# Performance work log

Hardware: AMD Instinct MI355X
Metric: run time of the kernel (lower is better)

Reference implementation:

```python
import jax, jax.numpy as jnp
import numpy as np

H = 512      # hidden_size
DB = 128     # dim_B
DC = 16      # dim_C
N = 2048     # batch


def setup_inputs() -> dict:
    key = jax.random.key(0)
    ks = jax.random.split(key, 8)
    u = lambda k, shp: jax.random.uniform(k, shp, jnp.float32, -0.1, 0.1)
    return {
        "input_data": jax.random.normal(ks[0], (N, H), jnp.float32),
        "W1": u(ks[1], (H, 2 * H)), "b1": jnp.zeros((2 * H,), jnp.float32),
        "W2": u(ks[2], (2 * H, 3 * H)), "b2": jnp.zeros((3 * H,), jnp.float32),
        "Wh": u(ks[3], (3 * H, 3 * H)), "bh": jnp.zeros((3 * H,), jnp.float32),
        "W3": u(ks[4], (3 * H, 2 * H)), "b3": jnp.zeros((2 * H,), jnp.float32),
        "W4": u(ks[5], (2 * H, H)), "b4": jnp.zeros((H,), jnp.float32),
        "Wo": u(ks[6], (H + DB, 1)), "bo": jnp.zeros((1,), jnp.float32),
        "T": jax.random.normal(ks[7], (H, DB * DC), jnp.float32),
    }


def _minibatch_disc(Ms):
    # Ms: [N, B, C]. out[i, b] = sum_j exp(-sum_c |Ms[i,b,c]-Ms[j,b,c]|)
    # Sequential map over B keeps the [N, N, C] intermediate bounded.
    def per_b(m):  # m: [N, C]
        d = jnp.sum(jnp.abs(m[:, None, :] - m[None, :, :]), axis=-1)  # [N, N]
        return jnp.sum(jnp.exp(-d), axis=1)  # [N]
    return jax.lax.map(per_b, jnp.transpose(Ms, (1, 0, 2))).T  # [N, B]


def reference(input_data, W1, b1, W2, b2, Wh, bh, W3, b3, W4, b4, Wo, bo, T):
    x = jax.nn.relu(input_data @ W1 + b1)
    x = jax.nn.relu(x @ W2 + b2)
    x = jax.nn.relu(x @ Wh + bh)  # dropout(p=0) == identity
    x = jax.nn.relu(x @ W3 + b3)
    feature = jax.nn.relu(x @ W4 + b4)          # [N, H]
    Ms = (feature @ T).reshape(-1, DB, DC)      # [N, B, C]
    out_T = _minibatch_disc(Ms)                 # [N, B]
    logits = jnp.concatenate([feature, out_T], axis=1) @ Wo + bo
    return feature, jax.nn.sigmoid(logits)
```

## Files before the change

### kernel.cpp

```cpp
#include <hip/hip_runtime.h>
#include <hip/hip_bf16.h>
#include <math.h>

#define NROWS 2048
#define HD 512
#define DBx 128

typedef __attribute__((ext_vector_type(8)))  short bf16x8;
typedef __attribute__((ext_vector_type(4)))  float f32x4;
typedef __attribute__((ext_vector_type(16))) float f32x16;

__device__ inline unsigned pack2_bf16(float a, float b) {
    union { __hip_bfloat162 h; unsigned u; } cv;
    cv.h = __float22bfloat162_rn(make_float2(a, b));
    return cv.u;
}
__device__ inline unsigned short pack1_bf16(float a) {
    union { __hip_bfloat16 h; unsigned short u; } cv;
    cv.h = __float2bfloat16(a);
    return cv.u;
}

__global__ __launch_bounds__(256) void conv_bf16_kernel(const float* __restrict__ in,
                                                        unsigned short* __restrict__ out,
                                                        int n4) {
    for (int idx = blockIdx.x * 256 + threadIdx.x; idx < n4; idx += gridDim.x * 256) {
        const float4 v = *reinterpret_cast<const float4*>(in + (size_t)idx * 4);
        uint2 o;
        o.x = pack2_bf16(v.x, v.y);
        o.y = pack2_bf16(v.z, v.w);
        *reinterpret_cast<uint2*>(out + (size_t)idx * 4) = o;
    }
}

struct TransArgs {
    const float* src[6];
    unsigned short* dst[6];
    int K[6], M[6], t0[6];
};

__global__ __launch_bounds__(256) void trans_all_kernel(TransArgs a) {
    const int id = blockIdx.x;
    int m = 0;
    #pragma unroll
    for (int q = 1; q < 6; ++q) if (id >= a.t0[q]) m = q;
    const int local = id - a.t0[m];
    const int M = a.M[m], K = a.K[m];
    const int ntm = M >> 5;
    const int mt = local % ntm;
    const int kt = local / ntm;
    const float* W = a.src[m];
    unsigned short* Wt = a.dst[m];

    __shared__ float tile[32][33];
    const int t  = threadIdx.x;
    const int tr = t >> 3;
    const int tc = t & 7;
    const int k0 = kt * 32;
    const int m0 = mt * 32;

    const float4 v = *reinterpret_cast<const float4*>(&W[(size_t)(k0 + tr) * M + m0 + tc * 4]);
    tile[tr][tc * 4 + 0] = v.x;
    tile[tr][tc * 4 + 1] = v.y;
    tile[tr][tc * 4 + 2] = v.z;
    tile[tr][tc * 4 + 3] = v.w;
    __syncthreads();

    const float x = tile[tc * 4 + 0][tr];
    const float y = tile[tc * 4 + 1][tr];
    const float z = tile[tc * 4 + 2][tr];
    const float w = tile[tc * 4 + 3][tr];
    uint2 o;
    o.x = pack2_bf16(x, y);
    o.y = pack2_bf16(z, w);
    *reinterpret_cast<uint2*>(&Wt[(size_t)(m0 + tr) * K + k0 + tc * 4]) = o;
}

template<int WRITE_BF16, int WRITE_F32, int RELU, int BIAS, int MSB>
__global__ __launch_bounds__(256) void gemm64_kernel(const unsigned short* __restrict__ Abf,
                                                     const unsigned short* __restrict__ Bt,
                                                     const float* __restrict__ bias,
                                                     unsigned short* __restrict__ Cbf,
                                                     float* __restrict__ Cf,
                                                     int K, int M) {
    __shared__ unsigned short As[2][64 * 64];
    __shared__ unsigned short Bs[2][64 * 64];

    const int t    = threadIdx.x;
    const int lane = t & 63;
    const int wv   = t >> 6;
    const int wm   = wv & 1;
    const int wn   = wv >> 1;
    const int row0 = blockIdx.y * 64;
    const int col0 = blockIdx.x * 64;
    const int gl_r = lane >> 3;
    const int gl_c = lane & 7;

    f32x4 acc[2][2] = {};

    auto STAGE = [&](int bufi, int kt) {
        #pragma unroll
        for (int q = 0; q < 2; ++q) {
            const int r = wv * 16 + q * 8 + gl_r;
            const unsigned short* srcA = Abf + (size_t)(row0 + r) * K + kt + 8 * (gl_c ^ (r & 7));
            __builtin_amdgcn_global_load_lds(
                (const __attribute__((address_space(1))) void*)srcA,
                (__attribute__((address_space(3))) void*)(&As[bufi][(wv * 16 + q * 8) * 64]),
                16, 0, 0);
            const unsigned short* srcB = Bt + (size_t)(col0 + r) * K + kt + 8 * (gl_c ^ (r & 7));
            __builtin_amdgcn_global_load_lds(
                (const __attribute__((address_space(1))) void*)srcB,
                (__attribute__((address_space(3))) void*)(&Bs[bufi][(wv * 16 + q * 8) * 64]),
                16, 0, 0);
        }
    };

    const int nkt = K >> 6;
    STAGE(0, 0);
    __syncthreads();
    int buf = 0;
    for (int kt = 0; kt < nkt; ++kt) {
        if (kt + 1 < nkt) STAGE(buf ^ 1, (kt + 1) * 64);
        const int lm = lane & 15;
        const int kg = lane >> 4;
        #pragma unroll
        for (int ks = 0; ks < 2; ++ks) {
            bf16x8 af[2], bfr[2];
            #pragma unroll
            for (int fi = 0; fi < 2; ++fi) {
                const int r  = wm * 32 + fi * 16 + lm;
                const int ch = (kg + 4 * ks) ^ (r & 7);
                af[fi] = *reinterpret_cast<const bf16x8*>((const char*)&As[buf][0] + r * 128 + ch * 16);
            }
            #pragma unroll
            for (int fj = 0; fj < 2; ++fj) {
                const int n  = wn * 32 + fj * 16 + lm;
                const int ch = (kg + 4 * ks) ^ (n & 7);
                bfr[fj] = *reinterpret_cast<const bf16x8*>((const char*)&Bs[buf][0] + n * 128 + ch * 16);
            }
            #pragma unroll
            for (int fi = 0; fi < 2; ++fi)
                #pragma unroll
                for (int fj = 0; fj < 2; ++fj)
                    acc[fi][fj] = __builtin_amdgcn_mfma_f32_16x16x32_bf16(
                        af[fi], bfr[fj], acc[fi][fj], 0, 0, 0);
        }
        __syncthreads();
        buf ^= 1;
    }

    const int lm = lane & 15;
    const int lq = lane >> 4;
    #pragma unroll
    for (int fj = 0; fj < 2; ++fj) {
        const int col = col0 + wn * 32 + fj * 16 + lm;
        const float bv = BIAS ? bias[col] : 0.f;
        #pragma unroll
        for (int fi = 0; fi < 2; ++fi) {
            #pragma unroll
            for (int r = 0; r < 4; ++r) {
                const int row = row0 + wm * 32 + fi * 16 + lq * 4 + r;
                float v = acc[fi][fj][r] + bv;
                if (RELU) v = fmaxf(v, 0.f);
                if (WRITE_F32)  Cf[(size_t)row * M + col] = v;
                if (WRITE_BF16) {
                    if (MSB)
                        Cbf[(size_t)(col >> 4) * (NROWS * 16) + (size_t)row * 16 + (col & 15)] = pack1_bf16(v);
                    else
                        Cbf[(size_t)row * M + col] = pack1_bf16(v);
                }
            }
        }
    }
}

__global__ __launch_bounds__(256) void norms_kernel(const float* __restrict__ Ms,
                                                    float* __restrict__ nrm,
                                                    float* __restrict__ oT) {
    const int g = blockIdx.x * 256 + threadIdx.x;
    const int i = g >> 7;
    const int b = g & 127;
    const float* p = Ms + (size_t)i * 2048 + b * 16;
    float s = 0.f;
    #pragma unroll
    for (int c = 0; c < 16; c += 4) {
        const float4 v = *reinterpret_cast<const float4*>(p + c);
        s += v.x * v.x + v.y * v.y + v.z * v.z + v.w * v.w;
    }
    nrm[(size_t)b * 2048 + i] = 0.495f * s;
    oT[g] = 0.f;
}

__global__ __launch_bounds__(512) void mbdisc32_kernel(const float* __restrict__ Ms,
                                                       const unsigned short* __restrict__ Msb,
                                                       const float* __restrict__ nrm,
                                                       float* __restrict__ outT) {
    extern __shared__ char smem[];
    float* Nlds = (float*)(smem + 32768);

    const int t    = threadIdx.x;
    const int lane = t & 63;
    const int w    = t >> 6;
    const int b    = blockIdx.y;
    const int jh   = blockIdx.z;
    const int cl   = lane & 31;
    const int hk   = lane >> 5;
    const int jbase = jh * 1024;

    const unsigned short* Mb = Msb + (size_t)b * NROWS * 16;
    const float* nb = nrm + (size_t)b * NROWS;

    #pragma unroll
    for (int q = 0; q < 4; ++q) {
        const int slot = q * 512 + t;
        const int h = slot >> 10, jj = slot & 1023;
        const unsigned short* src = Mb + (size_t)(jbase + jj) * 16 + h * 8;
        __builtin_amdgcn_global_load_lds(
            (const __attribute__((address_space(1))) void*)src,
            (__attribute__((address_space(3))) void*)(smem + (size_t)(q * 512 + w * 64) * 16),
            16, 0, 0);
    }
    if (w < 4) {
        const float* src = nb + jbase + (w * 64 + lane) * 4;
        __builtin_amdgcn_global_load_lds(
            (const __attribute__((address_space(1))) void*)src,
            (__attribute__((address_space(3))) void*)(smem + 32768 + (size_t)(w * 64) * 16),
            16, 0, 0);
    }

    bf16x8 afc[4];
    #pragma unroll
    for (int ic = 0; ic < 4; ++ic) {
        const int i0 = blockIdx.x * 1024 + w * 128 + ic * 32;
        afc[ic] = *reinterpret_cast<const bf16x8*>(Mb + (size_t)(i0 + cl) * 16 + hk * 8);
    }
    __syncthreads();

    const char* mrow = smem + hk * 16384;

    #pragma unroll
    for (int ic = 0; ic < 4; ++ic) {
        const int i0 = blockIdx.x * 1024 + w * 128 + ic * 32;
        const bf16x8 af = afc[ic];

        f32x16 cI;
        #pragma unroll
        for (int q = 0; q < 4; ++q) {
            const float4 v = *reinterpret_cast<const float4*>(nb + i0 + 4 * hk + 8 * q);
            cI[4 * q + 0] = 725.f - v.x; cI[4 * q + 1] = 725.f - v.y;
            cI[4 * q + 2] = 725.f - v.z; cI[4 * q + 3] = 725.f - v.w;
        }

        #pragma unroll 2
        for (int j0 = 0; j0 < 1024; j0 += 64) {
            const float nj0 = Nlds[j0 + cl];
            const float nj1 = Nlds[j0 + 32 + cl];
            const bf16x8 b0 = *reinterpret_cast<const bf16x8*>(mrow + (size_t)(j0 + cl) * 16);
            const bf16x8 b1 = *reinterpret_cast<const bf16x8*>(mrow + (size_t)(j0 + 32 + cl) * 16);
            const f32x16 a0 = __builtin_amdgcn_mfma_f32_32x32x16_bf16(af, b0, cI, 0, 0, 0);
            const f32x16 a1 = __builtin_amdgcn_mfma_f32_32x32x16_bf16(af, b1, cI, 0, 0, 0);

            float x0 = fmaxf(fmaxf(a0[0], a0[1]), fmaxf(a0[2], a0[3]));
            float x1 = fmaxf(fmaxf(a0[4], a0[5]), fmaxf(a0[6], a0[7]));
            float x2 = fmaxf(fmaxf(a0[8], a0[9]), fmaxf(a0[10], a0[11]));
            float x3 = fmaxf(fmaxf(a0[12], a0[13]), fmaxf(a0[14], a0[15]));
            const float mx0 = fmaxf(fmaxf(x0, x1), fmaxf(x2, x3));
            float y0 = fmaxf(fmaxf(a1[0], a1[1]), fmaxf(a1[2], a1[3]));
            float y1 = fmaxf(fmaxf(a1[4], a1[5]), fmaxf(a1[6], a1[7]));
            float y2 = fmaxf(fmaxf(a1[8], a1[9]), fmaxf(a1[10], a1[11]));
            float y3 = fmaxf(fmaxf(a1[12], a1[13]), fmaxf(a1[14], a1[15]));
            const float mx1 = fmaxf(fmaxf(y0, y1), fmaxf(y2, y3));

            if (__any(fmaxf(mx0 - nj0, mx1 - nj1) > 0.f)) {
                #pragma unroll
                for (int r = 0; r < 16; ++r) {
                    if (a0[r] > nj0) {
                        const int i = i0 + (r & 3) + 8 * (r >> 2) + 4 * hk;
                        const int j = jbase + j0 + cl;
                        const float* pi = Ms + (size_t)i * 2048 + b * 16;
                        const float* pj = Ms + (size_t)j * 2048 + b * 16;
                        float s = 0.f;
                        #pragma unroll
                        for (int cc = 0; cc < 16; cc += 4) {
                            const float4 x = *reinterpret_cast<const float4*>(pi + cc);
                            const float4 y = *reinterpret_cast<const float4*>(pj + cc);
                            s += (fabsf(x.x - y.x) + fabsf(x.y - y.y)) +
                                 (fabsf(x.z - y.z) + fabsf(x.w - y.w));
                        }
                        atomicAdd(&outT[(size_t)i * DBx + b], __expf(-s));
                    }
                }
                #pragma unroll
                for (int r = 0; r < 16; ++r) {
                    if (a1[r] > nj1) {
                        const int i = i0 + (r & 3) + 8 * (r >> 2) + 4 * hk;
                        const int j = jbase + j0 + 32 + cl;
                        const float* pi = Ms + (size_t)i * 2048 + b * 16;
                        const float* pj = Ms + (size_t)j * 2048 + b * 16;
                        float s = 0.f;
                        #pragma unroll
                        for (int cc = 0; cc < 16; cc += 4) {
                            const float4 x = *reinterpret_cast<const float4*>(pi + cc);
                            const float4 y = *reinterpret_cast<const float4*>(pj + cc);
                            s += (fabsf(x.x - y.x) + fabsf(x.y - y.y)) +
                                 (fabsf(x.z - y.z) + fabsf(x.w - y.w));
                        }
                        atomicAdd(&outT[(size_t)i * DBx + b], __expf(-s));
                    }
                }
            }
        }
    }
}

__global__ __launch_bounds__(256) void logits_kernel(const float* __restrict__ feat,
                                                     const float* __restrict__ outT,
                                                     const float* __restrict__ Wo,
                                                     const float* __restrict__ bo,
                                                     float* __restrict__ out2) {
    const int row = blockIdx.x;
    const int t   = threadIdx.x;
    float p = 0.f;
    for (int k = t; k < HD + DBx; k += 256) {
        const float x = (k < HD) ? feat[(size_t)row * HD + k]
                                 : outT[(size_t)row * DBx + (k - HD)];
        p += x * Wo[k];
    }
    #pragma unroll
    for (int off = 32; off; off >>= 1) p += __shfl_down(p, off, 64);
    __shared__ float ws[4];
    if ((t & 63) == 0) ws[t >> 6] = p;
    __syncthreads();
    if (t == 0) {
        const float s = ws[0] + ws[1] + ws[2] + ws[3] + bo[0];
        out2[row] = 1.f / (1.f + __expf(-s));
    }
}

extern "C" void kernel_launch(void* const* d_in, const int* in_sizes, int n_in,
                              void* d_out, int out_size, void* d_ws, size_t ws_size,
                              hipStream_t stream) {
    const float* input = (const float*)d_in[0];
    const float* W1 = (const float*)d_in[1];
    const float* b1 = (const float*)d_in[2];
    const float* W2 = (const float*)d_in[3];
    const float* b2 = (const float*)d_in[4];
    const float* Wh = (const float*)d_in[5];
    const float* bh = (const float*)d_in[6];
    const float* W3 = (const float*)d_in[7];
    const float* b3 = (const float*)d_in[8];
    const float* W4 = (const float*)d_in[9];
    const float* b4 = (const float*)d_in[10];
    const float* Wo = (const float*)d_in[11];
    const float* bo = (const float*)d_in[12];
    const float* T  = (const float*)d_in[13];

    unsigned short* inbf  = (unsigned short*)d_ws;
    unsigned short* W1t   = inbf  + (size_t)2048 * 512;
    unsigned short* W2t   = W1t   + (size_t)1024 * 512;
    unsigned short* Wht   = W2t   + (size_t)1536 * 1024;
    unsigned short* W3t   = Wht   + (size_t)1536 * 1536;
    unsigned short* W4t   = W3t   + (size_t)1024 * 1536;
    unsigned short* Tt    = W4t   + (size_t)512 * 1024;
    unsigned short* slabA = Tt    + (size_t)2048 * 512;
    unsigned short* slabB = slabA + (size_t)2048 * 1536;
    float* Ms  = (float*)(slabB + (size_t)2048 * 1536);
    float* oT  = Ms + (size_t)2048 * 2048;
    float* nrm = oT + (size_t)2048 * 128;
    unsigned short* Msb = inbf;

    unsigned short* x1bf   = slabA;
    unsigned short* x2bf   = slabB;
    unsigned short* x3bf   = slabA;
    unsigned short* x4bf   = slabB;
    unsigned short* featbf = slabA;

    float* feat = (float*)d_out;
    float* out2 = feat + (size_t)NROWS * HD;

    const dim3 blk(256);

    conv_bf16_kernel<<<1024, blk, 0, stream>>>(input, inbf, 2048 * 512 / 4);

    TransArgs ta;
    ta.src[0] = W1; ta.dst[0] = W1t; ta.K[0] =  512; ta.M[0] = 1024; ta.t0[0] = 0;
    ta.src[1] = W2; ta.dst[1] = W2t; ta.K[1] = 1024; ta.M[1] = 1536; ta.t0[1] = 512;
    ta.src[2] = Wh; ta.dst[2] = Wht; ta.K[2] = 1536; ta.M[2] = 1536; ta.t0[2] = 2048;
    ta.src[3] = W3; ta.dst[3] = W3t; ta.K[3] = 1536; ta.M[3] = 1024; ta.t0[3] = 4352;
    ta.src[4] = W4; ta.dst[4] = W4t; ta.K[4] = 1024; ta.M[4] =  512; ta.t0[4] = 5888;
    ta.src[5] = T;  ta.dst[5] = Tt;  ta.K[5] =  512; ta.M[5] = 2048; ta.t0[5] = 6400;
    trans_all_kernel<<<7424, blk, 0, stream>>>(ta);

    gemm64_kernel<1, 0, 1, 1, 0><<<dim3(1024 / 64, 32), blk, 0, stream>>>(inbf, W1t, b1, x1bf, nullptr, 512, 1024);
    gemm64_kernel<1, 0, 1, 1, 0><<<dim3(1536 / 64, 32), blk, 0, stream>>>(x1bf, W2t, b2, x2bf, nullptr, 1024, 1536);
    gemm64_kernel<1, 0, 1, 1, 0><<<dim3(1536 / 64, 32), blk, 0, stream>>>(x2bf, Wht, bh, x3bf, nullptr, 1536, 1536);
    gemm64_kernel<1, 0, 1, 1, 0><<<dim3(1024 / 64, 32), blk, 0, stream>>>(x3bf, W3t, b3, x4bf, nullptr, 1536, 1024);
    gemm64_kernel<1, 1, 1, 1, 0><<<dim3( 512 / 64, 32), blk, 0, stream>>>(x4bf, W4t, b4, featbf, feat, 1024, 512);
    gemm64_kernel<1, 1, 0, 0, 1><<<dim3(2048 / 64, 32), blk, 0, stream>>>(featbf, Tt, nullptr, Msb, Ms, 512, 2048);

    norms_kernel<<<1024, blk, 0, stream>>>(Ms, nrm, oT);
    mbdisc32_kernel<<<dim3(2, 128, 2), dim3(512), 36864, stream>>>(Ms, Msb, nrm, oT);

    logits_kernel<<<NROWS, blk, 0, stream>>>(feat, oT, Wo, bo, out2);
}
```

Baseline: 262.1 us.

## Exploit pairwise symmetry in minibatch discrimination and fuse input conversion into transpose

```diff
diff --git a/kernel.cpp b/kernel.cpp
--- a/kernel.cpp
+++ b/kernel.cpp
@@ -19,18 +19,6 @@
     union { __hip_bfloat16 h; unsigned short u; } cv;
     cv.h = __float2bfloat16(a);
     return cv.u;
-}
-
-__global__ __launch_bounds__(256) void conv_bf16_kernel(const float* __restrict__ in,
-                                                        unsigned short* __restrict__ out,
-                                                        int n4) {
-    for (int idx = blockIdx.x * 256 + threadIdx.x; idx < n4; idx += gridDim.x * 256) {
-        const float4 v = *reinterpret_cast<const float4*>(in + (size_t)idx * 4);
-        uint2 o;
-        o.x = pack2_bf16(v.x, v.y);
-        o.y = pack2_bf16(v.z, v.w);
-        *reinterpret_cast<uint2*>(out + (size_t)idx * 4) = o;
-    }
 }
 
 struct TransArgs {
@@ -38,9 +26,22 @@
     unsigned short* dst[6];
     int K[6], M[6], t0[6];
 };
-
-__global__ __launch_bounds__(256) void trans_all_kernel(TransArgs a) {
+#define TRANS_BLOCKS 7424
+#define CONV_BLOCKS  1024
+
+__global__ __launch_bounds__(256) void trans_all_kernel(TransArgs a,
+                                                        const float* __restrict__ cin,
+                                                        unsigned short* __restrict__ cout) {
     const int id = blockIdx.x;
+    if (id >= TRANS_BLOCKS) {
+        const int idx = (id - TRANS_BLOCKS) * 256 + threadIdx.x;
+        const float4 v = *reinterpret_cast<const float4*>(cin + (size_t)idx * 4);
+        uint2 o;
+        o.x = pack2_bf16(v.x, v.y);
+        o.y = pack2_bf16(v.z, v.w);
+        *reinterpret_cast<uint2*>(cout + (size_t)idx * 4) = o;
+        return;
+    }
     int m = 0;
     #pragma unroll
     for (int q = 1; q < 6; ++q) if (id >= a.t0[q]) m = q;
@@ -188,7 +189,7 @@
         s += v.x * v.x + v.y * v.y + v.z * v.z + v.w * v.w;
     }
     nrm[(size_t)b * 2048 + i] = 0.495f * s;
-    oT[g] = 0.f;
+    oT[g] = 1.0f;
 }
 
 __global__ __launch_bounds__(512) void mbdisc32_kernel(const float* __restrict__ Ms,
@@ -202,9 +203,12 @@
     const int lane = t & 63;
     const int w    = t >> 6;
     const int b    = blockIdx.y;
-    const int jh   = blockIdx.z;
+    const int bx   = blockIdx.x;
+    const int bz   = blockIdx.z;
     const int cl   = lane & 31;
     const int hk   = lane >> 5;
+    const int diag = (bx == bz);
+    const int jh   = bx | bz;
     const int jbase = jh * 1024;
 
     const unsigned short* Mb = Msb + (size_t)b * NROWS * 16;
@@ -228,84 +232,77 @@
             16, 0, 0);
     }
 
+    int qs[4];
+    int nq;
+    if (diag) {
+        qs[0] = w; qs[1] = 15 - w; qs[2] = 16 + w; qs[3] = 31 - w; nq = 4;
+    } else {
+        const int o = (bx == 1) ? 16 : 0;
+        qs[0] = o + 2 * w; qs[1] = o + 2 * w + 1; nq = 2;
+        qs[2] = qs[0]; qs[3] = qs[1];
+    }
+    const int ibase = diag ? bx * 1024 : 0;
+
     bf16x8 afc[4];
     #pragma unroll
-    for (int ic = 0; ic < 4; ++ic) {
-        const int i0 = blockIdx.x * 1024 + w * 128 + ic * 32;
-        afc[ic] = *reinterpret_cast<const bf16x8*>(Mb + (size_t)(i0 + cl) * 16 + hk * 8);
+    for (int qi = 0; qi < 4; ++qi) {
+        const int i0 = ibase + qs[qi] * 32;
+        afc[qi] = *reinterpret_cast<const bf16x8*>(Mb + (size_t)(i0 + cl) * 16 + hk * 8);
     }
     __syncthreads();
 
     const char* mrow = smem + hk * 16384;
 
-    #pragma unroll
-    for (int ic = 0; ic < 4; ++ic) {
-        const int i0 = blockIdx.x * 1024 + w * 128 + ic * 32;
-        const bf16x8 af = afc[ic];
+    for (int qi = 0; qi < nq; ++qi) {
+        const int q  = qs[qi];
+        const int i0 = ibase + q * 32;
+        const bf16x8 af = afc[qi];
 
         f32x16 cI;
         #pragma unroll
-        for (int q = 0; q < 4; ++q) {
-            const float4 v = *reinterpret_cast<const float4*>(nb + i0 + 4 * hk + 8 * q);
-            cI[4 * q + 0] = 725.f - v.x; cI[4 * q + 1] = 725.f - v.y;
-            cI[4 * q + 2] = 725.f - v.z; cI[4 * q + 3] = 725.f - v.w;
+        for (int p = 0; p < 4; ++p) {
+            const float4 v = *reinterpret_cast<const float4*>(nb + i0 + 4 * hk + 8 * p);
+            cI[4 * p + 0] = 725.f - v.x; cI[4 * p + 1] = 725.f - v.y;
+            cI[4 * p + 2] = 725.f - v.z; cI[4 * p + 3] = 725.f - v.w;
         }
 
+        const int jt0 = diag ? q : 0;
         #pragma unroll 2
-        for (int j0 = 0; j0 < 1024; j0 += 64) {
-            const float nj0 = Nlds[j0 + cl];
-            const float nj1 = Nlds[j0 + 32 + cl];
-            const bf16x8 b0 = *reinterpret_cast<const bf16x8*>(mrow + (size_t)(j0 + cl) * 16);
-            const bf16x8 b1 = *reinterpret_cast<const bf16x8*>(mrow + (size_t)(j0 + 32 + cl) * 16);
-            const f32x16 a0 = __builtin_amdgcn_mfma_f32_32x32x16_bf16(af, b0, cI, 0, 0, 0);
-            const f32x16 a1 = __builtin_amdgcn_mfma_f32_32x32x16_bf16(af, b1, cI, 0, 0, 0);
-
-            float x0 = fmaxf(fmaxf(a0[0], a0[1]), fmaxf(a0[2], a0[3]));
-            float x1 = fmaxf(fmaxf(a0[4], a0[5]), fmaxf(a0[6], a0[7]));
-            float x2 = fmaxf(fmaxf(a0[8], a0[9]), fmaxf(a0[10], a0[11]));
-            float x3 = fmaxf(fmaxf(a0[12], a0[13]), fmaxf(a0[14], a0[15]));
-            const float mx0 = fmaxf(fmaxf(x0, x1), fmaxf(x2, x3));
-            float y0 = fmaxf(fmaxf(a1[0], a1[1]), fmaxf(a1[2], a1[3]));
-            float y1 = fmaxf(fmaxf(a1[4], a1[5]), fmaxf(a1[6], a1[7]));
-            float y2 = fmaxf(fmaxf(a1[8], a1[9]), fmaxf(a1[10], a1[11]));
-            float y3 = fmaxf(fmaxf(a1[12], a1[13]), fmaxf(a1[14], a1[15]));
-            const float mx1 = fmaxf(fmaxf(y0, y1), fmaxf(y2, y3));
-
-            if (__any(fmaxf(mx0 - nj0, mx1 - nj1) > 0.f)) {
+        for (int jt = jt0; jt < 32; ++jt) {
+            const int j0 = jt * 32;
+            const float njv  = Nlds[j0 + cl];
+            const bf16x8 bfr = *reinterpret_cast<const bf16x8*>(mrow + (size_t)(j0 + cl) * 16);
+            const f32x16 acc = __builtin_amdgcn_mfma_f32_32x32x16_bf16(af, bfr, cI, 0, 0, 0);
+
+            const float p0 = fmaxf(fmaxf(acc[0],  acc[1]),  acc[2]);
+            const float p1 = fmaxf(fmaxf(acc[3],  acc[4]),  acc[5]);
+            const float p2 = fmaxf(fmaxf(acc[6],  acc[7]),  acc[8]);
+            const float p3 = fmaxf(fmaxf(acc[9],  acc[10]), acc[11]);
+            const float p4 = fmaxf(fmaxf(acc[12], acc[13]), acc[14]);
+            const float mx = fmaxf(fmaxf(fmaxf(p0, p1), acc[15]),
+                                   fmaxf(fmaxf(p2, p3), p4));
+
+            if (__any(mx > njv)) {
                 #pragma unroll
                 for (int r = 0; r < 16; ++r) {
-                    if (a0[r] > nj0) {
+                    if (acc[r] > njv) {
                         const int i = i0 + (r & 3) + 8 * (r >> 2) + 4 * hk;
                         const int j = jbase + j0 + cl;
-                        const float* pi = Ms + (size_t)i * 2048 + b * 16;
-                        const float* pj = Ms + (size_t)j * 2048 + b * 16;
-                        float s = 0.f;
-                        #pragma unroll
-                        for (int cc = 0; cc < 16; cc += 4) {
-                            const float4 x = *reinterpret_cast<const float4*>(pi + cc);
-                            const float4 y = *reinterpret_cast<const float4*>(pj + cc);
-                            s += (fabsf(x.x - y.x) + fabsf(x.y - y.y)) +
-                                 (fabsf(x.z - y.z) + fabsf(x.w - y.w));
+                        if (j > i) {
+                            const float* pi = Ms + (size_t)i * 2048 + b * 16;
+                            const float* pj = Ms + (size_t)j * 2048 + b * 16;
+                            float s = 0.f;
+                            #pragma unroll
+                            for (int cc = 0; cc < 16; cc += 4) {
+                                const float4 x = *reinterpret_cast<const float4*>(pi + cc);
+                                const float4 y = *reinterpret_cast<const float4*>(pj + cc);
+                                s += (fabsf(x.x - y.x) + fabsf(x.y - y.y)) +
+                                     (fabsf(x.z - y.z) + fabsf(x.w - y.w));
+                            }
+                            const float e = __expf(-s);
+                            atomicAdd(&outT[(size_t)i * DBx + b], e);
+                            atomicAdd(&outT[(size_t)j * DBx + b], e);
                         }
-                        atomicAdd(&outT[(size_t)i * DBx + b], __expf(-s));
-                    }
-                }
-                #pragma unroll
-                for (int r = 0; r < 16; ++r) {
-                    if (a1[r] > nj1) {
-                        const int i = i0 + (r & 3) + 8 * (r >> 2) + 4 * hk;
-                        const int j = jbase + j0 + 32 + cl;
-                        const float* pi = Ms + (size_t)i * 2048 + b * 16;
-                        const float* pj = Ms + (size_t)j * 2048 + b * 16;
-                        float s = 0.f;
-                        #pragma unroll
-                        for (int cc = 0; cc < 16; cc += 4) {
-                            const float4 x = *reinterpret_cast<const float4*>(pi + cc);
-                            const float4 y = *reinterpret_cast<const float4*>(pj + cc);
-                            s += (fabsf(x.x - y.x) + fabsf(x.y - y.y)) +
-                                 (fabsf(x.z - y.z) + fabsf(x.w - y.w));
-                        }
-                        atomicAdd(&outT[(size_t)i * DBx + b], __expf(-s));
                     }
                 }
             }
@@ -380,8 +377,6 @@
 
     const dim3 blk(256);
 
-    conv_bf16_kernel<<<1024, blk, 0, stream>>>(input, inbf, 2048 * 512 / 4);
-
     TransArgs ta;
     ta.src[0] = W1; ta.dst[0] = W1t; ta.K[0] =  512; ta.M[0] = 1024; ta.t0[0] = 0;
     ta.src[1] = W2; ta.dst[1] = W2t; ta.K[1] = 1024; ta.M[1] = 1536; ta.t0[1] = 512;
@@ -389,7 +384,7 @@
     ta.src[3] = W3; ta.dst[3] = W3t; ta.K[3] = 1536; ta.M[3] = 1024; ta.t0[3] = 4352;
     ta.src[4] = W4; ta.dst[4] = W4t; ta.K[4] = 1024; ta.M[4] =  512; ta.t0[4] = 5888;
     ta.src[5] = T;  ta.dst[5] = Tt;  ta.K[5] =  512; ta.M[5] = 2048; ta.t0[5] = 6400;
-    trans_all_kernel<<<7424, blk, 0, stream>>>(ta);
+    trans_all_kernel<<<TRANS_BLOCKS + CONV_BLOCKS, blk, 0, stream>>>(ta, input, inbf);
 
     gemm64_kernel<1, 0, 1, 1, 0><<<dim3(1024 / 64, 32), blk, 0, stream>>>(inbf, W1t, b1, x1bf, nullptr, 512, 1024);
     gemm64_kernel<1, 0, 1, 1, 0><<<dim3(1536 / 64, 32), blk, 0, stream>>>(x1bf, W2t, b2, x2bf, nullptr, 1024, 1536);
```

Result: faster. 229.8 us (-12.3%).
